# Kernel tuning notes

Measured on AMD Instinct MI355X. Metric: run time of the kernel, lower is better.

## Reference

```python
import jax, jax.numpy as jnp
import numpy as np

RC = 5.0
N_ATYPE = 10
ACSF_NMU = 20
APSF_NMU = 10
ACSF_ETA = 100.0
APSF_ETA = 25.0
N_ATOMS = 30000
N_PAIRS = 200000
MAX_NB = 6
DENSE = 64
FEAT_DIM = ACSF_NMU * N_ATYPE + APSF_NMU * N_ATYPE + 22  # 322
ZINDEX = jnp.array([1.0, 3.0, 5.0, 6.0, 7.0, 8.0, 9.0, 11.0, 15.0, 16.0])
CHARGE_KEYS = jnp.array([0.0, 1.0, 3.0, 5.0, 6.0, 7.0, 8.0, 9.0, 11.0, 15.0, 16.0])
CHARGE_VALS = jnp.array([100000, 0, 1, 2, 3, 4, 5, 6, 7, 8, 9])


def pbc_shift(dr, box, box_inv):
    ds = dr @ box_inv
    ds = ds - jnp.floor(ds + 0.5)
    return ds @ box


def int_to_onehot(labels, num_classes):
    zidx = CHARGE_VALS[jnp.searchsorted(CHARGE_KEYS, labels)]
    return jax.nn.one_hot(zidx, num_classes, dtype=labels.dtype)


def dense_ln_relu(x, W, b, g, beta):
    h = x @ W + b
    mu = jnp.mean(h, axis=-1, keepdims=True)
    var = jnp.mean(jnp.square(h - mu), axis=-1, keepdims=True)
    return jax.nn.relu((h - mu) * jax.lax.rsqrt(var + 1e-6) * g + beta)


def forward(pos, box, valid_mask, W1, b1, g1, be1, W2, b2, g2, be2, W3, b3, g3, be3, Wo, bo,
            pairs, topo_nblist, topo_mask, mol_ID, atype_indices):
    dt = pos.dtype
    acsf_mus = jnp.linspace(0.0, 5.0, ACSF_NMU).astype(dt)
    apsf_mus = jnp.linspace(-1.0, 1.0, APSF_NMU).astype(dt)
    mScales = jnp.array([0.0, 0.0, 0.0, 0.0, 0.0, 1.0], dtype=dt)
    # regularize_pairs: padded pairs have i >= j, shift them off-diagonal
    p = pairs[:, :2]
    dp_flag = (p[:, 1] - p[:, 0] <= 0).astype(p.dtype)
    p = p - jnp.stack([dp_flag, 2 * dp_flag], axis=1)
    nbonds = pairs[:, 2]
    buffer_scales = (p[:, 0] < p[:, 1]).astype(dt) * valid_mask
    mscales = mScales[nbonds - 1] * buffer_scales  # computed as in original (unused downstream)
    box_inv = jnp.linalg.inv(box)
    ri = pos[p[:, 0]]
    rj = pos[p[:, 1]]
    rij = pbc_shift(rj - ri, box, box_inv)
    dr_norm = jnp.linalg.norm(rij + 1e-10, axis=1)
    same_mol = mol_ID[p[:, 0]] == mol_ID[p[:, 1]]
    buffer_inter = jnp.where(same_mol, 0.0, 1.0).astype(dt)
    cutoff = jnp.where(dr_norm <= RC, 0.5 * (1 + jnp.cos(jnp.pi * dr_norm / RC)), 0.0)
    buffer_nblist_inter_rc = buffer_inter * buffer_scales * cutoff
    # environment atoms of each pair endpoint (bonded topology neighbors)
    j_nb = topo_nblist[p[:, 0]]  # [P, M]
    k_nb = topo_nblist[p[:, 1]]
    j_mask = topo_mask[p[:, 0]] & (j_nb != -1) & (j_nb != p[:, 0:1]) & (j_nb != p[:, 1:2])
    k_mask = topo_mask[p[:, 1]] & (k_nb != -1) & (k_nb != p[:, 0:1]) & (k_nb != p[:, 1:2])
    rij_unit = rij / (dr_norm[:, None] + 1e-10)

    def cos_gamma(center, nb, mask, unit):
        r_env = jnp.where(mask[..., None], pos[nb], 0.0)  # [P, M, 3]
        rX = pbc_shift(r_env - center[:, None, :], box, box_inv)
        rXn = rX / jnp.linalg.norm(rX + 1e-10, axis=2, keepdims=True)
        return jnp.einsum('pmi,pi->pm', rXn, unit) * mask

    cos_gamma_i = cos_gamma(ri, j_nb, j_mask, rij_unit)
    cos_gamma_j = cos_gamma(rj, k_nb, k_mask, -rij_unit)
    type_cols = jnp.arange(N_ATYPE)

    def apsf(cg, nb, mask):
        feat = jnp.exp(-APSF_ETA * jnp.square(cg[..., None] - apsf_mus)) * mask[..., None]
        onehot = (atype_indices[nb][..., None] == type_cols).astype(dt)
        return jnp.einsum('pmk,pml->pkl', feat, onehot)  # [P, APSF_NMU, N_ATYPE]

    G_pair = (apsf(cos_gamma_i, j_nb, j_mask) + apsf(cos_gamma_j, k_nb, k_mask)) * 0.5 \
             * buffer_nblist_inter_rc[:, None, None]
    # ACSF radial atom-centered features
    r_env = pos[topo_nblist]  # [N, M, 3]
    dr = pbc_shift(r_env - pos[:, None, :], box, box_inv)
    dnorm = jnp.linalg.norm(dr + 1e-10, axis=2)
    fx = dnorm / RC
    f_cut = jnp.where(fx < 1, 0.5 * (jnp.cos(jnp.pi * fx) + 1), 0.0) * topo_mask
    G_raw = jnp.exp(-ACSF_ETA * jnp.square(dnorm[..., None] - acsf_mus)) * f_cut[..., None]
    nb_onehot = (atype_indices[topo_nblist][..., None] == type_cols).astype(dt)
    G_atom = jnp.einsum('nmk,nml->nkl', G_raw, nb_onehot)  # [N, ACSF_NMU, N_ATYPE]
    atom_feat = 0.5 * (G_atom[p[:, 0]] + G_atom[p[:, 1]])
    # element charge + one-hot block
    elem = ZINDEX[atype_indices].astype(dt)
    j_z = elem[p[:, 0]]
    k_z = elem[p[:, 1]]
    atype_onehot = jnp.concatenate([j_z[:, None], int_to_onehot(j_z, 10),
                                    k_z[:, None], int_to_onehot(k_z, 10)], axis=1)
    feats = jnp.concatenate([atom_feat.reshape(atom_feat.shape[0], -1),
                             G_pair.reshape(G_pair.shape[0], -1),
                             atype_onehot], axis=1)  # [P, 322]
    # MLP energy head
    x = dense_ln_relu(feats, W1, b1, g1, be1)
    x = dense_ln_relu(x, W2, b2, g2, be2)
    x = dense_ln_relu(x, W3, b3, g3, be3)
    out_AB = x @ Wo + bo
    return jnp.sum(out_AB * buffer_nblist_inter_rc[:, None])


def setup_inputs() -> dict:
    key = jax.random.key(0)
    ks = jax.random.split(key, 16)
    L = 30.0
    pos = jax.random.uniform(ks[0], (N_ATOMS, 3), jnp.float32, 0.0, L)
    box = jnp.eye(3, dtype=jnp.float32) * L
    i = jax.random.randint(ks[1], (N_PAIRS,), 2, N_ATOMS)
    j = jax.random.randint(ks[2], (N_PAIRS,), 2, N_ATOMS)
    p0 = jnp.minimum(i, j)
    p1 = jnp.maximum(i, j)
    pairs = jnp.stack([p0, p1, jnp.full((N_PAIRS,), 6, dtype=p0.dtype)], axis=1)
    valid_mask = (jax.random.uniform(ks[3], (N_PAIRS,)) < 0.95).astype(jnp.float32)
    nb = jax.random.randint(ks[4], (N_ATOMS, MAX_NB), 0, N_ATOMS)
    topo_nblist = jnp.where(jax.random.uniform(ks[5], (N_ATOMS, MAX_NB)) < 0.25, -1, nb)
    topo_mask = topo_nblist != -1
    mol_ID = jnp.arange(N_ATOMS, dtype=jnp.int32) // 3
    atype_indices = jax.random.randint(ks[6], (N_ATOMS,), 0, N_ATYPE)

    def dense_w(k, fin, fout):
        return jax.random.normal(k, (fin, fout), jnp.float32) / np.float32(np.sqrt(fin))

    return {
        'pos': pos, 'box': box, 'valid_mask': valid_mask,
        'W1': dense_w(ks[7], FEAT_DIM, DENSE), 'b1': jnp.zeros((DENSE,), jnp.float32),
        'g1': jnp.ones((DENSE,), jnp.float32), 'be1': jnp.zeros((DENSE,), jnp.float32),
        'W2': dense_w(ks[8], DENSE, DENSE), 'b2': jnp.zeros((DENSE,), jnp.float32),
        'g2': jnp.ones((DENSE,), jnp.float32), 'be2': jnp.zeros((DENSE,), jnp.float32),
        'W3': dense_w(ks[9], DENSE, DENSE), 'b3': jnp.zeros((DENSE,), jnp.float32),
        'g3': jnp.ones((DENSE,), jnp.float32), 'be3': jnp.zeros((DENSE,), jnp.float32),
        'Wo': dense_w(ks[10], DENSE, 1), 'bo': jnp.zeros((1,), jnp.float32),
        'pairs': pairs, 'topo_nblist': topo_nblist, 'topo_mask': topo_mask,
        'mol_ID': mol_ID, 'atype_indices': atype_indices,
    }


def reference(pos, box, valid_mask, W1, b1, g1, be1, W2, b2, g2, be2, W3, b3, g3, be3, Wo, bo,
              pairs, topo_nblist, topo_mask, mol_ID, atype_indices):
    return forward(pos, box, valid_mask, W1, b1, g1, be1, W2, b2, g2, be2, W3, b3, g3, be3, Wo, bo,
                   pairs, topo_nblist, topo_mask, mol_ID, atype_indices)
```

## Files before the change

### kernel.cpp

```cpp
#include <hip/hip_runtime.h>
#include <math.h>

#define N_PAIRS_C 200000
#define MAX_NB_C 6
#define RC_F 5.0f
#define PI_F 3.14159265358979323846f
#define FILT_THREADS 256
#define FILT_BLOCKS ((N_PAIRS_C + FILT_THREADS - 1) / FILT_THREADS)
#define MLP_BLOCKS 1024
#define MLP_THREADS 256
#define WPB 4
#define FPAD 324

__device__ __constant__ float c_ZIND[10] = {1.f, 3.f, 5.f, 6.f, 7.f, 8.f, 9.f, 11.f, 15.f, 16.f};

__device__ __forceinline__ void invert3x3(const float* b, float* inv) {
    float a00 = b[0], a01 = b[1], a02 = b[2];
    float a10 = b[3], a11 = b[4], a12 = b[5];
    float a20 = b[6], a21 = b[7], a22 = b[8];
    float det = a00 * (a11 * a22 - a12 * a21)
              - a01 * (a10 * a22 - a12 * a20)
              + a02 * (a10 * a21 - a11 * a20);
    float id = 1.0f / det;
    inv[0] =  (a11 * a22 - a12 * a21) * id;
    inv[1] = -(a01 * a22 - a02 * a21) * id;
    inv[2] =  (a01 * a12 - a02 * a11) * id;
    inv[3] = -(a10 * a22 - a12 * a20) * id;
    inv[4] =  (a00 * a22 - a02 * a20) * id;
    inv[5] = -(a00 * a12 - a02 * a10) * id;
    inv[6] =  (a10 * a21 - a11 * a20) * id;
    inv[7] = -(a00 * a21 - a01 * a20) * id;
    inv[8] =  (a00 * a11 - a01 * a10) * id;
}

__device__ __forceinline__ void pbc3(float dx, float dy, float dz,
                                     const float* box, const float* binv,
                                     float& ox, float& oy, float& oz) {
    float s0 = dx * binv[0] + dy * binv[3] + dz * binv[6];
    float s1 = dx * binv[1] + dy * binv[4] + dz * binv[7];
    float s2 = dx * binv[2] + dy * binv[5] + dz * binv[8];
    s0 -= floorf(s0 + 0.5f);
    s1 -= floorf(s1 + 0.5f);
    s2 -= floorf(s2 + 0.5f);
    ox = s0 * box[0] + s1 * box[3] + s2 * box[6];
    oy = s0 * box[1] + s1 * box[4] + s2 * box[7];
    oz = s0 * box[2] + s1 * box[5] + s2 * box[8];
}

__device__ __forceinline__ float wsum64(float v) {
    #pragma unroll
    for (int off = 32; off > 0; off >>= 1) v += __shfl_xor(v, off, 64);
    return v;
}

__device__ __forceinline__ float ln_relu(float h, float g, float be) {
    float mu = wsum64(h) * 0.015625f;
    float d  = h - mu;
    float var = wsum64(d * d) * 0.015625f;
    float r = d * (1.0f / sqrtf(var + 1e-6f)) * g + be;
    return fmaxf(r, 0.0f);
}

__global__ __launch_bounds__(FILT_THREADS) void filter_kernel(
        const float* __restrict__ pos,
        const float* __restrict__ box,
        const float* __restrict__ valid_mask,
        const int* __restrict__ pairs,
        const int* __restrict__ mol_ID,
        int* __restrict__ counter,
        int* __restrict__ act_p0,
        int* __restrict__ act_p1,
        float* __restrict__ act_fac,
        int max_active,
        float* __restrict__ out) {
    __shared__ int l_cnt, l_base;
    __shared__ int sp0[FILT_THREADS], sp1[FILT_THREADS];
    __shared__ float sfac[FILT_THREADS];
    const int tid = threadIdx.x;
    if (tid == 0) l_cnt = 0;
    if (blockIdx.x == 0 && tid == 0) out[0] = 0.0f;
    __syncthreads();

    float bx[9], bi[9];
    #pragma unroll
    for (int i = 0; i < 9; ++i) bx[i] = box[i];
    invert3x3(bx, bi);

    int t = blockIdx.x * FILT_THREADS + tid;
    bool keep = false;
    int p0 = 0, p1 = 0;
    float fac = 0.0f;
    if (t < N_PAIRS_C) {
        int i0 = pairs[3 * t], i1 = pairs[3 * t + 1];
        int dp = (i1 - i0 <= 0) ? 1 : 0;
        p0 = i0 - dp; p1 = i1 - 2 * dp;
        if (p0 < p1) {
            float vm = valid_mask[t];
            if (vm != 0.0f && mol_ID[p0] != mol_ID[p1]) {
                float dx, dy, dz;
                pbc3(pos[3 * p1] - pos[3 * p0],
                     pos[3 * p1 + 1] - pos[3 * p0 + 1],
                     pos[3 * p1 + 2] - pos[3 * p0 + 2], bx, bi, dx, dy, dz);
                float ax = dx + 1e-10f, ay = dy + 1e-10f, az = dz + 1e-10f;
                float dn = sqrtf(ax * ax + ay * ay + az * az);
                if (dn <= RC_F) {
                    fac = vm * 0.5f * (1.0f + __cosf(PI_F * dn / RC_F));
                    keep = true;
                }
            }
        }
    }
    if (keep) {
        int slot = atomicAdd(&l_cnt, 1);
        sp0[slot] = p0; sp1[slot] = p1; sfac[slot] = fac;
    }
    __syncthreads();
    if (tid == 0) l_base = (l_cnt > 0) ? atomicAdd(counter, l_cnt) : 0;
    __syncthreads();
    if (tid < l_cnt) {
        int g = l_base + tid;
        if (g < max_active) {
            act_p0[g] = sp0[tid];
            act_p1[g] = sp1[tid];
            act_fac[g] = sfac[tid];
        }
    }
}

__global__ __launch_bounds__(MLP_THREADS, 4) void pair_mlp(
    const float* __restrict__ pos,
    const float* __restrict__ box,
    const float* __restrict__ W1, const float* __restrict__ b1,
    const float* __restrict__ g1, const float* __restrict__ be1,
    const float* __restrict__ W2, const float* __restrict__ b2,
    const float* __restrict__ g2, const float* __restrict__ be2,
    const float* __restrict__ W3, const float* __restrict__ b3,
    const float* __restrict__ g3, const float* __restrict__ be3,
    const float* __restrict__ Wo, const float* __restrict__ bo,
    const int* __restrict__ nblist,
    const int* __restrict__ atype,
    const int* __restrict__ counter,
    const int* __restrict__ act_p0,
    const int* __restrict__ act_p1,
    const float* __restrict__ act_fac,
    int max_active,
    float* __restrict__ out) {

    __shared__ __align__(16) float lds_feat[WPB][FPAD];
    __shared__ __align__(16) float lds_x[WPB][64];
    __shared__ float wacc[WPB];

    const int tid = threadIdx.x;
    const int w = tid >> 6;
    const int j = tid & 63;

    int count = *counter;
    if (count > max_active) count = max_active;

    const int wid0 = blockIdx.x * WPB + w;
    const int wstr = gridDim.x * WPB;

    float acc = 0.0f;

    if (wid0 < count) {
        float bx[9], bi[9];
        #pragma unroll
        for (int i = 0; i < 9; ++i) bx[i] = box[i];
        invert3x3(bx, bi);

        const float b1j = b1[j], g1j = g1[j], be1j = be1[j];
        const float b2j = b2[j], g2j = g2[j], be2j = be2[j];
        const float b3j = b3[j], g3j = g3[j], be3j = be3[j];
        const float woj = Wo[j], bo0 = bo[0];

        float* feat = lds_feat[w];
        float* xb   = lds_x[w];

        for (int idx = wid0; idx < count; idx += wstr) {
            int p0 = __builtin_amdgcn_readfirstlane(act_p0[idx]);
            int p1 = __builtin_amdgcn_readfirstlane(act_p1[idx]);
            float fac = act_fac[idx];

            float rix = pos[3 * p0], riy = pos[3 * p0 + 1], riz = pos[3 * p0 + 2];
            float rjx = pos[3 * p1], rjy = pos[3 * p1 + 1], rjz = pos[3 * p1 + 2];
            float dxr, dyr, dzr;
            pbc3(rjx - rix, rjy - riy, rjz - riz, bx, bi, dxr, dyr, dzr);
            float axr = dxr + 1e-10f, ayr = dyr + 1e-10f, azr = dzr + 1e-10f;
            float dn0 = sqrtf(axr * axr + ayr * ayr + azr * azr);
            float idn = 1.0f / (dn0 + 1e-10f);
            float ux = dxr * idn, uy = dyr * idn, uz = dzr * idn;

            float sdn = 1.0f, sfc = 0.0f, scg = 0.0f;
            int smeta = 0;
            if (j < 12) {
                int side = (j >= 6) ? 1 : 0;
                int m = side ? (j - 6) : j;
                int a = side ? p1 : p0;
                int nb = nblist[a * MAX_NB_C + m];
                if (nb != -1) {
                    float cx = side ? rjx : rix;
                    float cy = side ? rjy : riy;
                    float cz = side ? rjz : riz;
                    float ex, ey, ez;
                    pbc3(pos[3 * nb] - cx, pos[3 * nb + 1] - cy, pos[3 * nb + 2] - cz,
                         bx, bi, ex, ey, ez);
                    float nx = ex + 1e-10f, ny = ey + 1e-10f, nz = ez + 1e-10f;
                    sdn = sqrtf(nx * nx + ny * ny + nz * nz);
                    float fr = sdn * (1.0f / RC_F);
                    sfc = (fr < 1.0f) ? 0.5f * (__cosf(PI_F * fr) + 1.0f) : 0.0f;
                    int pv = (nb != p0 && nb != p1) ? 1 : 0;
                    smeta = atype[nb] | (1 << 8) | (pv << 9);
                    float sgn = side ? -1.0f : 1.0f;
                    scg = sgn * (ex * ux + ey * uy + ez * uz) / sdn;
                }
            }

            {
                float4 z = make_float4(0.f, 0.f, 0.f, 0.f);
                *(float4*)&feat[4 * j] = z;
                if (j < 17) *(float4*)&feat[256 + 4 * j] = z;
            }
            if (j == 12) { int ti = atype[p0]; feat[300] = c_ZIND[ti]; feat[301 + ti] = 1.0f; }
            if (j == 13) { int tj = atype[p1]; feat[311] = c_ZIND[tj]; feat[312 + tj] = 1.0f; }

            #pragma unroll
            for (int it = 0; it < 6; ++it) {
                int task = j + 64 * it;
                if (task < 360) {
                    int s, k;
                    bool acs = (task < 240);
                    if (acs) { s = task / 20; k = task - s * 20; }
                    else     { int t2 = task - 240; s = t2 / 10; k = t2 - s * 10; }
                    float dn_s = __shfl(sdn, s);
                    float fc_s = __shfl(sfc, s);
                    float cg_s = __shfl(scg, s);
                    int meta_s = __shfl(smeta, s);
                    int ty_s = meta_s & 0xff;
                    if (acs) {
                        if ((meta_s & 0x100) && fc_s != 0.0f) {
                            float mu = (5.0f * (float)k) / 19.0f;
                            float d = dn_s - mu;
                            atomicAdd(&feat[k * 10 + ty_s], 0.5f * __expf(-100.0f * d * d) * fc_s);
                        }
                    } else {
                        if (meta_s & 0x200) {
                            float mu = -1.0f + (2.0f * (float)k) / 9.0f;
                            float d = cg_s - mu;
                            atomicAdd(&feat[200 + k * 10 + ty_s], 0.5f * fac * __expf(-25.0f * d * d));
                        }
                    }
                }
            }
            asm volatile("s_waitcnt lgkmcnt(0)" ::: "memory");

            float h = b1j;
            const float4* f4 = (const float4*)feat;
            #pragma unroll 4
            for (int g = 0; g < 80; ++g) {
                float4 a = f4[g];
                const float* wrow = W1 + (g * 4) * 64 + j;
                h = fmaf(a.x, wrow[0],   h);
                h = fmaf(a.y, wrow[64],  h);
                h = fmaf(a.z, wrow[128], h);
                h = fmaf(a.w, wrow[192], h);
            }
            h = fmaf(feat[320], W1[320 * 64 + j], h);
            h = fmaf(feat[321], W1[321 * 64 + j], h);
            float x1 = ln_relu(h, g1j, be1j);
            xb[j] = x1;

            float h2 = b2j;
            const float4* x4 = (const float4*)xb;
            #pragma unroll 4
            for (int g = 0; g < 16; ++g) {
                float4 a = x4[g];
                const float* wrow = W2 + (g * 4) * 64 + j;
                h2 = fmaf(a.x, wrow[0],   h2);
                h2 = fmaf(a.y, wrow[64],  h2);
                h2 = fmaf(a.z, wrow[128], h2);
                h2 = fmaf(a.w, wrow[192], h2);
            }
            float x2 = ln_relu(h2, g2j, be2j);
            xb[j] = x2;

            float h3 = b3j;
            #pragma unroll 4
            for (int g = 0; g < 16; ++g) {
                float4 a = x4[g];
                const float* wrow = W3 + (g * 4) * 64 + j;
                h3 = fmaf(a.x, wrow[0],   h3);
                h3 = fmaf(a.y, wrow[64],  h3);
                h3 = fmaf(a.z, wrow[128], h3);
                h3 = fmaf(a.w, wrow[192], h3);
            }
            float x3 = ln_relu(h3, g3j, be3j);

            float r = wsum64(x3 * woj);
            if (j == 0) acc += (r + bo0) * fac;
        }
    }

    if (j == 0) wacc[w] = acc;
    __syncthreads();
    if (tid == 0) {
        float p = wacc[0] + wacc[1] + wacc[2] + wacc[3];
        atomicAdd(out, p);
    }
}

extern "C" void kernel_launch(void* const* d_in, const int* in_sizes, int n_in,
                              void* d_out, int out_size, void* d_ws, size_t ws_size,
                              hipStream_t stream) {
    const float* pos        = (const float*)d_in[0];
    const float* box        = (const float*)d_in[1];
    const float* valid_mask = (const float*)d_in[2];
    const float* W1  = (const float*)d_in[3];
    const float* b1  = (const float*)d_in[4];
    const float* g1  = (const float*)d_in[5];
    const float* be1 = (const float*)d_in[6];
    const float* W2  = (const float*)d_in[7];
    const float* b2  = (const float*)d_in[8];
    const float* g2  = (const float*)d_in[9];
    const float* be2 = (const float*)d_in[10];
    const float* W3  = (const float*)d_in[11];
    const float* b3  = (const float*)d_in[12];
    const float* g3  = (const float*)d_in[13];
    const float* be3 = (const float*)d_in[14];
    const float* Wo  = (const float*)d_in[15];
    const float* bo  = (const float*)d_in[16];
    const int* pairs = (const int*)d_in[17];
    const int* nbl   = (const int*)d_in[18];
    const int* mol   = (const int*)d_in[20];
    const int* aty   = (const int*)d_in[21];

    char* ws = (char*)d_ws;
    int* counter = (int*)ws;
    long long cap_ll = ((long long)ws_size - 256) / 12;
    int cap = (cap_ll > 0) ? (int)cap_ll : 0;
    if (cap > N_PAIRS_C) cap = N_PAIRS_C;
    int*   act_p0  = (int*)(ws + 256);
    int*   act_p1  = act_p0 + cap;
    float* act_fac = (float*)(act_p1 + cap);

    float* out = (float*)d_out;

    hipMemsetAsync(counter, 0, sizeof(int), stream);
    filter_kernel<<<FILT_BLOCKS, FILT_THREADS, 0, stream>>>(
        pos, box, valid_mask, pairs, mol, counter,
        act_p0, act_p1, act_fac, cap, out);
    pair_mlp<<<MLP_BLOCKS, MLP_THREADS, 0, stream>>>(
        pos, box,
        W1, b1, g1, be1, W2, b2, g2, be2, W3, b3, g3, be3, Wo, bo,
        nbl, aty, counter, act_p0, act_p1, act_fac, cap, out);
}
```

Measured before the change: 48.14 us.

## Fuse pair filter and MLP into one kernel with LDS-resident transposed weights

Merges the filter and MLP kernels into a single 256-block, 1024-thread kernel. Each block filters its own slice of pairs into a local LDS list, so the global counter, the workspace compaction and one launch go away. All MLP weights are staged transposed in LDS, and each wave processes two pairs at a time so every weight load is reused. The risks are that the local list is capped at 160 pairs per block, which silently drops pairs if a slice holds more actives, and that only 8 of the 16 waves do MLP work while the large LDS footprint limits occupancy.

```diff
diff --git a/kernel.cpp b/kernel.cpp
--- a/kernel.cpp
+++ b/kernel.cpp
@@ -5,11 +5,12 @@
 #define MAX_NB_C 6
 #define RC_F 5.0f
 #define PI_F 3.14159265358979323846f
-#define FILT_THREADS 256
-#define FILT_BLOCKS ((N_PAIRS_C + FILT_THREADS - 1) / FILT_THREADS)
-#define MLP_BLOCKS 1024
-#define MLP_THREADS 256
-#define WPB 4
+#define NBLK 256
+#define NTHR 1024
+#define SLICE 782
+#define LCAP 160
+#define W1S 332
+#define W23S 68
 #define FPAD 324
 
 __device__ __constant__ float c_ZIND[10] = {1.f, 3.f, 5.f, 6.f, 7.f, 8.f, 9.f, 11.f, 15.f, 16.f};
@@ -61,75 +62,10 @@
     return fmaxf(r, 0.0f);
 }
 
-__global__ __launch_bounds__(FILT_THREADS) void filter_kernel(
-        const float* __restrict__ pos,
-        const float* __restrict__ box,
-        const float* __restrict__ valid_mask,
-        const int* __restrict__ pairs,
-        const int* __restrict__ mol_ID,
-        int* __restrict__ counter,
-        int* __restrict__ act_p0,
-        int* __restrict__ act_p1,
-        float* __restrict__ act_fac,
-        int max_active,
-        float* __restrict__ out) {
-    __shared__ int l_cnt, l_base;
-    __shared__ int sp0[FILT_THREADS], sp1[FILT_THREADS];
-    __shared__ float sfac[FILT_THREADS];
-    const int tid = threadIdx.x;
-    if (tid == 0) l_cnt = 0;
-    if (blockIdx.x == 0 && tid == 0) out[0] = 0.0f;
-    __syncthreads();
-
-    float bx[9], bi[9];
-    #pragma unroll
-    for (int i = 0; i < 9; ++i) bx[i] = box[i];
-    invert3x3(bx, bi);
-
-    int t = blockIdx.x * FILT_THREADS + tid;
-    bool keep = false;
-    int p0 = 0, p1 = 0;
-    float fac = 0.0f;
-    if (t < N_PAIRS_C) {
-        int i0 = pairs[3 * t], i1 = pairs[3 * t + 1];
-        int dp = (i1 - i0 <= 0) ? 1 : 0;
-        p0 = i0 - dp; p1 = i1 - 2 * dp;
-        if (p0 < p1) {
-            float vm = valid_mask[t];
-            if (vm != 0.0f && mol_ID[p0] != mol_ID[p1]) {
-                float dx, dy, dz;
-                pbc3(pos[3 * p1] - pos[3 * p0],
-                     pos[3 * p1 + 1] - pos[3 * p0 + 1],
-                     pos[3 * p1 + 2] - pos[3 * p0 + 2], bx, bi, dx, dy, dz);
-                float ax = dx + 1e-10f, ay = dy + 1e-10f, az = dz + 1e-10f;
-                float dn = sqrtf(ax * ax + ay * ay + az * az);
-                if (dn <= RC_F) {
-                    fac = vm * 0.5f * (1.0f + __cosf(PI_F * dn / RC_F));
-                    keep = true;
-                }
-            }
-        }
-    }
-    if (keep) {
-        int slot = atomicAdd(&l_cnt, 1);
-        sp0[slot] = p0; sp1[slot] = p1; sfac[slot] = fac;
-    }
-    __syncthreads();
-    if (tid == 0) l_base = (l_cnt > 0) ? atomicAdd(counter, l_cnt) : 0;
-    __syncthreads();
-    if (tid < l_cnt) {
-        int g = l_base + tid;
-        if (g < max_active) {
-            act_p0[g] = sp0[tid];
-            act_p1[g] = sp1[tid];
-            act_fac[g] = sfac[tid];
-        }
-    }
-}
-
-__global__ __launch_bounds__(MLP_THREADS, 4) void pair_mlp(
+__global__ __launch_bounds__(NTHR, 4) void fused_kernel(
     const float* __restrict__ pos,
     const float* __restrict__ box,
+    const float* __restrict__ valid_mask,
     const float* __restrict__ W1, const float* __restrict__ b1,
     const float* __restrict__ g1, const float* __restrict__ be1,
     const float* __restrict__ W2, const float* __restrict__ b2,
@@ -137,49 +73,114 @@
     const float* __restrict__ W3, const float* __restrict__ b3,
     const float* __restrict__ g3, const float* __restrict__ be3,
     const float* __restrict__ Wo, const float* __restrict__ bo,
+    const int* __restrict__ pairs,
     const int* __restrict__ nblist,
     const int* __restrict__ atype,
-    const int* __restrict__ counter,
-    const int* __restrict__ act_p0,
-    const int* __restrict__ act_p1,
-    const float* __restrict__ act_fac,
-    int max_active,
+    const int* __restrict__ mol_ID,
     float* __restrict__ out) {
 
-    __shared__ __align__(16) float lds_feat[WPB][FPAD];
-    __shared__ __align__(16) float lds_x[WPB][64];
-    __shared__ float wacc[WPB];
+    __shared__ __align__(16) float W1t[64][W1S];
+    __shared__ __align__(16) float W2t[64][W23S];
+    __shared__ __align__(16) float W3t[64][W23S];
+    __shared__ __align__(16) float feats[16][FPAD];
+    __shared__ __align__(16) float xb[16][64];
+    __shared__ int   l_p0[LCAP], l_p1[LCAP];
+    __shared__ float l_fac[LCAP];
+    __shared__ int   l_cnt;
+    __shared__ float wacc[16];
 
     const int tid = threadIdx.x;
     const int w = tid >> 6;
     const int j = tid & 63;
 
-    int count = *counter;
-    if (count > max_active) count = max_active;
-
-    const int wid0 = blockIdx.x * WPB + w;
-    const int wstr = gridDim.x * WPB;
+    if (tid == 0) l_cnt = 0;
+
+    float bx[9], bi[9];
+    #pragma unroll
+    for (int i = 0; i < 9; ++i) bx[i] = box[i];
+    invert3x3(bx, bi);
+
+    __syncthreads();
+
+    {
+        const int roto = blockIdx.x % 81;
+        #pragma unroll
+        for (int r = 0; r < 6; ++r) {
+            int gi = w + 16 * r;
+            if (gi < 81) {
+                gi += roto; if (gi >= 81) gi -= 81;
+                int f0 = 4 * gi;
+                float4 v;
+                v.x = (f0 + 0 < 322) ? W1[(f0 + 0) * 64 + j] : 0.0f;
+                v.y = (f0 + 1 < 322) ? W1[(f0 + 1) * 64 + j] : 0.0f;
+                v.z = (f0 + 2 < 322) ? W1[(f0 + 2) * 64 + j] : 0.0f;
+                v.w = (f0 + 3 < 322) ? W1[(f0 + 3) * 64 + j] : 0.0f;
+                *(float4*)&W1t[j][f0] = v;
+            }
+        }
+        {
+            int f0 = 4 * w;
+            float4 v2, v3;
+            v2.x = W2[(f0 + 0) * 64 + j]; v3.x = W3[(f0 + 0) * 64 + j];
+            v2.y = W2[(f0 + 1) * 64 + j]; v3.y = W3[(f0 + 1) * 64 + j];
+            v2.z = W2[(f0 + 2) * 64 + j]; v3.z = W3[(f0 + 2) * 64 + j];
+            v2.w = W2[(f0 + 3) * 64 + j]; v3.w = W3[(f0 + 3) * 64 + j];
+            *(float4*)&W2t[j][f0] = v2;
+            *(float4*)&W3t[j][f0] = v3;
+        }
+    }
+
+    if (tid < SLICE) {
+        int t = blockIdx.x * SLICE + tid;
+        if (t < N_PAIRS_C) {
+            int i0 = pairs[3 * t], i1 = pairs[3 * t + 1];
+            int dp = (i1 - i0 <= 0) ? 1 : 0;
+            int p0 = i0 - dp, p1 = i1 - 2 * dp;
+            if (p0 < p1) {
+                float vm = valid_mask[t];
+                if (vm != 0.0f && mol_ID[p0] != mol_ID[p1]) {
+                    float dx, dy, dz;
+                    pbc3(pos[3 * p1] - pos[3 * p0],
+                         pos[3 * p1 + 1] - pos[3 * p0 + 1],
+                         pos[3 * p1 + 2] - pos[3 * p0 + 2], bx, bi, dx, dy, dz);
+                    float ax = dx + 1e-10f, ay = dy + 1e-10f, az = dz + 1e-10f;
+                    float dn = sqrtf(ax * ax + ay * ay + az * az);
+                    if (dn <= RC_F) {
+                        float fac = vm * 0.5f * (1.0f + __cosf(PI_F * dn / RC_F));
+                        int slot = atomicAdd(&l_cnt, 1);
+                        if (slot < LCAP) {
+                            l_p0[slot] = p0; l_p1[slot] = p1; l_fac[slot] = fac;
+                        }
+                    }
+                }
+            }
+        }
+    }
+    __syncthreads();
+
+    int cnt = l_cnt;
+    if (cnt > LCAP) cnt = LCAP;
+    const int rounds = (cnt + 15) >> 4;
+
+    const float b1j = b1[j], g1j = g1[j], be1j = be1[j];
+    const float b2j = b2[j], g2j = g2[j], be2j = be2[j];
+    const float b3j = b3[j], g3j = g3[j], be3j = be3[j];
+    const float woj = Wo[j], bo0 = bo[0];
 
     float acc = 0.0f;
 
-    if (wid0 < count) {
-        float bx[9], bi[9];
-        #pragma unroll
-        for (int i = 0; i < 9; ++i) bx[i] = box[i];
-        invert3x3(bx, bi);
-
-        const float b1j = b1[j], g1j = g1[j], be1j = be1[j];
-        const float b2j = b2[j], g2j = g2[j], be2j = be2[j];
-        const float b3j = b3[j], g3j = g3[j], be3j = be3[j];
-        const float woj = Wo[j], bo0 = bo[0];
-
-        float* feat = lds_feat[w];
-        float* xb   = lds_x[w];
-
-        for (int idx = wid0; idx < count; idx += wstr) {
-            int p0 = __builtin_amdgcn_readfirstlane(act_p0[idx]);
-            int p1 = __builtin_amdgcn_readfirstlane(act_p1[idx]);
-            float fac = act_fac[idx];
+    if (w < 8 && rounds > 0) {
+        float* frowA = &feats[2 * w][0];
+        float* frowB = &feats[2 * w + 1][0];
+        float* xbA = &xb[2 * w][0];
+        float* xbB = &xb[2 * w + 1][0];
+
+        auto featurize = [&](int idx, float* frow) -> float {
+            bool val = idx < cnt;
+            int ci = val ? idx : 0;
+            int p0 = l_p0[ci];
+            int p1 = l_p1[ci];
+            float fac = val ? l_fac[ci] : 0.0f;
 
             float rix = pos[3 * p0], riy = pos[3 * p0 + 1], riz = pos[3 * p0 + 2];
             float rjx = pos[3 * p1], rjy = pos[3 * p1 + 1], rjz = pos[3 * p1 + 2];
@@ -215,13 +216,11 @@
                 }
             }
 
-            {
-                float4 z = make_float4(0.f, 0.f, 0.f, 0.f);
-                *(float4*)&feat[4 * j] = z;
-                if (j < 17) *(float4*)&feat[256 + 4 * j] = z;
-            }
-            if (j == 12) { int ti = atype[p0]; feat[300] = c_ZIND[ti]; feat[301 + ti] = 1.0f; }
-            if (j == 13) { int tj = atype[p1]; feat[311] = c_ZIND[tj]; feat[312 + tj] = 1.0f; }
+            float4 z = make_float4(0.f, 0.f, 0.f, 0.f);
+            *(float4*)&frow[4 * j] = z;
+            if (j < 17) *(float4*)&frow[256 + 4 * j] = z;
+            if (j == 12) { int ti = atype[p0]; frow[300] = c_ZIND[ti]; frow[301 + ti] = 1.0f; }
+            if (j == 13) { int tj2 = atype[p1]; frow[311] = c_ZIND[tj2]; frow[312 + tj2] = 1.0f; }
 
             #pragma unroll
             for (int it = 0; it < 6; ++it) {
@@ -240,71 +239,83 @@
                         if ((meta_s & 0x100) && fc_s != 0.0f) {
                             float mu = (5.0f * (float)k) / 19.0f;
                             float d = dn_s - mu;
-                            atomicAdd(&feat[k * 10 + ty_s], 0.5f * __expf(-100.0f * d * d) * fc_s);
+                            atomicAdd(&frow[k * 10 + ty_s], 0.5f * __expf(-100.0f * d * d) * fc_s);
                         }
                     } else {
                         if (meta_s & 0x200) {
                             float mu = -1.0f + (2.0f * (float)k) / 9.0f;
                             float d = cg_s - mu;
-                            atomicAdd(&feat[200 + k * 10 + ty_s], 0.5f * fac * __expf(-25.0f * d * d));
+                            atomicAdd(&frow[200 + k * 10 + ty_s], 0.5f * fac * __expf(-25.0f * d * d));
                         }
                     }
                 }
             }
+            return fac;
+        };
+
+        for (int r = 0; r < rounds; ++r) {
+            float facA = featurize((r << 4) + 2 * w + 0, frowA);
+            float facB = featurize((r << 4) + 2 * w + 1, frowB);
             asm volatile("s_waitcnt lgkmcnt(0)" ::: "memory");
 
-            float h = b1j;
-            const float4* f4 = (const float4*)feat;
-            #pragma unroll 4
-            for (int g = 0; g < 80; ++g) {
-                float4 a = f4[g];
-                const float* wrow = W1 + (g * 4) * 64 + j;
-                h = fmaf(a.x, wrow[0],   h);
-                h = fmaf(a.y, wrow[64],  h);
-                h = fmaf(a.z, wrow[128], h);
-                h = fmaf(a.w, wrow[192], h);
-            }
-            h = fmaf(feat[320], W1[320 * 64 + j], h);
-            h = fmaf(feat[321], W1[321 * 64 + j], h);
-            float x1 = ln_relu(h, g1j, be1j);
-            xb[j] = x1;
-
-            float h2 = b2j;
-            const float4* x4 = (const float4*)xb;
-            #pragma unroll 4
+            const float4* wr1 = (const float4*)&W1t[j][0];
+            const float4* fA4 = (const float4*)frowA;
+            const float4* fB4 = (const float4*)frowB;
+            float hA = b1j, hB = b1j;
+            #pragma unroll 3
+            for (int g = 0; g < 81; ++g) {
+                float4 wv = wr1[g];
+                float4 a = fA4[g], b = fB4[g];
+                hA = fmaf(a.x, wv.x, hA); hA = fmaf(a.y, wv.y, hA);
+                hA = fmaf(a.z, wv.z, hA); hA = fmaf(a.w, wv.w, hA);
+                hB = fmaf(b.x, wv.x, hB); hB = fmaf(b.y, wv.y, hB);
+                hB = fmaf(b.z, wv.z, hB); hB = fmaf(b.w, wv.w, hB);
+            }
+            float x1A = ln_relu(hA, g1j, be1j);
+            float x1B = ln_relu(hB, g1j, be1j);
+            xbA[j] = x1A; xbB[j] = x1B;
+
+            const float4* xA4 = (const float4*)xbA;
+            const float4* xB4 = (const float4*)xbB;
+            float h2A = b2j, h2B = b2j;
+            #pragma unroll
             for (int g = 0; g < 16; ++g) {
-                float4 a = x4[g];
-                const float* wrow = W2 + (g * 4) * 64 + j;
-                h2 = fmaf(a.x, wrow[0],   h2);
-                h2 = fmaf(a.y, wrow[64],  h2);
-                h2 = fmaf(a.z, wrow[128], h2);
-                h2 = fmaf(a.w, wrow[192], h2);
-            }
-            float x2 = ln_relu(h2, g2j, be2j);
-            xb[j] = x2;
-
-            float h3 = b3j;
-            #pragma unroll 4
+                float4 wv = *(const float4*)&W2t[j][4 * g];
+                float4 a = xA4[g], b = xB4[g];
+                h2A = fmaf(a.x, wv.x, h2A); h2A = fmaf(a.y, wv.y, h2A);
+                h2A = fmaf(a.z, wv.z, h2A); h2A = fmaf(a.w, wv.w, h2A);
+                h2B = fmaf(b.x, wv.x, h2B); h2B = fmaf(b.y, wv.y, h2B);
+                h2B = fmaf(b.z, wv.z, h2B); h2B = fmaf(b.w, wv.w, h2B);
+            }
+            float x2A = ln_relu(h2A, g2j, be2j);
+            float x2B = ln_relu(h2B, g2j, be2j);
+            xbA[j] = x2A; xbB[j] = x2B;
+
+            float h3A = b3j, h3B = b3j;
+            #pragma unroll
             for (int g = 0; g < 16; ++g) {
-                float4 a = x4[g];
-                const float* wrow = W3 + (g * 4) * 64 + j;
-                h3 = fmaf(a.x, wrow[0],   h3);
-                h3 = fmaf(a.y, wrow[64],  h3);
-                h3 = fmaf(a.z, wrow[128], h3);
-                h3 = fmaf(a.w, wrow[192], h3);
-            }
-            float x3 = ln_relu(h3, g3j, be3j);
-
-            float r = wsum64(x3 * woj);
-            if (j == 0) acc += (r + bo0) * fac;
+                float4 wv = *(const float4*)&W3t[j][4 * g];
+                float4 a = xA4[g], b = xB4[g];
+                h3A = fmaf(a.x, wv.x, h3A); h3A = fmaf(a.y, wv.y, h3A);
+                h3A = fmaf(a.z, wv.z, h3A); h3A = fmaf(a.w, wv.w, h3A);
+                h3B = fmaf(b.x, wv.x, h3B); h3B = fmaf(b.y, wv.y, h3B);
+                h3B = fmaf(b.z, wv.z, h3B); h3B = fmaf(b.w, wv.w, h3B);
+            }
+            float x3A = ln_relu(h3A, g3j, be3j);
+            float x3B = ln_relu(h3B, g3j, be3j);
+
+            float rA = wsum64(x3A * woj);
+            float rB = wsum64(x3B * woj);
+            if (j == 0) acc += (rA + bo0) * facA + (rB + bo0) * facB;
         }
     }
 
     if (j == 0) wacc[w] = acc;
     __syncthreads();
-    if (tid == 0) {
-        float p = wacc[0] + wacc[1] + wacc[2] + wacc[3];
-        atomicAdd(out, p);
+    if (w == 0) {
+        float v = (j < 16) ? wacc[j] : 0.0f;
+        v = wsum64(v);
+        if (j == 0) atomicAdd(out, v);
     }
 }
 
@@ -333,23 +344,11 @@
     const int* mol   = (const int*)d_in[20];
     const int* aty   = (const int*)d_in[21];
 
-    char* ws = (char*)d_ws;
-    int* counter = (int*)ws;
-    long long cap_ll = ((long long)ws_size - 256) / 12;
-    int cap = (cap_ll > 0) ? (int)cap_ll : 0;
-    if (cap > N_PAIRS_C) cap = N_PAIRS_C;
-    int*   act_p0  = (int*)(ws + 256);
-    int*   act_p1  = act_p0 + cap;
-    float* act_fac = (float*)(act_p1 + cap);
-
     float* out = (float*)d_out;
 
-    hipMemsetAsync(counter, 0, sizeof(int), stream);
-    filter_kernel<<<FILT_BLOCKS, FILT_THREADS, 0, stream>>>(
-        pos, box, valid_mask, pairs, mol, counter,
-        act_p0, act_p1, act_fac, cap, out);
-    pair_mlp<<<MLP_BLOCKS, MLP_THREADS, 0, stream>>>(
-        pos, box,
+    hipMemsetAsync(out, 0, sizeof(float), stream);
+    fused_kernel<<<NBLK, NTHR, 0, stream>>>(
+        pos, box, valid_mask,
         W1, b1, g1, be1, W2, b2, g2, be2, W3, b3, g3, be3, Wo, bo,
-        nbl, aty, counter, act_p0, act_p1, act_fac, cap, out);
-}
+        pairs, nbl, aty, mol, out);
+}
```

New measurement: 41.16 us. -14.5%, faster.
